# Kernel optimization log

Hardware: AMD Instinct MI355X
Metric: run time of the kernel (lower is better)

## Reference

```python
import jax, jax.numpy as jnp
import numpy as np

LN_EPS = 1e-5
LEAKY_SLOPE = 0.2

B, N_FEAT = 512, 8192
N_GROUPS, G, D = 512, 64, 128


def setup_inputs() -> dict:
    key = jax.random.key(0)
    k1, k2, k3 = jax.random.split(key, 3)
    x = jax.random.normal(k1, (B, N_FEAT), dtype=jnp.float32)
    idx = jax.random.randint(k2, (N_GROUPS, G), 0, N_FEAT)
    # per-group Linear weights, scaled like torch default init ~U(-1/sqrt(fan_in),...)
    W = jax.random.normal(k3, (N_GROUPS, G, D), dtype=jnp.float32) / jnp.sqrt(jnp.float32(G))
    b = jnp.zeros((N_GROUPS, D), dtype=jnp.float32)
    gamma = jnp.ones((D,), dtype=jnp.float32)   # shared LayerNorm affine (single nn.LayerNorm)
    beta = jnp.zeros((D,), dtype=jnp.float32)
    return {"x": x, "idx": idx, "W": W, "b": b, "gamma": gamma, "beta": beta}


def reference(x, idx, W, b, gamma, beta):
    # Gather each group's feature subset: [B, n_groups, G]
    xg = x[:, idx]
    # Grouped (block-diagonal) GEMM: per-group Linear -> [B, n_groups, D]
    h = jnp.einsum('bng,ngd->bnd', xg, W) + b
    # LeakyReLU(0.2)
    h = jnp.where(h >= 0, h, LEAKY_SLOPE * h)
    # Shared LayerNorm over last dim
    mu = jnp.mean(h, axis=-1, keepdims=True)
    c = h - mu
    var = jnp.mean(c * c, axis=-1, keepdims=True)
    out = c * jax.lax.rsqrt(var + LN_EPS) * gamma + beta
    # dropout treated as identity (deterministic/eval reference)
    return out  # matches torch.stack(output, dim=1): [B, n_groups, D]
```

## Files before the change

kernel.cpp:

```cpp
#include <hip/hip_runtime.h>
#include <stdint.h>

#define NB 512
#define NFEAT 8192
#define NG 512
#define GG 64
#define DD 128

typedef short bf16x8 __attribute__((ext_vector_type(8)));
typedef float f32x4 __attribute__((ext_vector_type(4)));
typedef unsigned int u32x4 __attribute__((ext_vector_type(4)));
typedef unsigned short u16;
typedef unsigned int u32;

__device__ __forceinline__ u16 f2bf(float f) {
  unsigned u = __builtin_bit_cast(unsigned, f);
  u += 0x7FFFu + ((u >> 16) & 1u);
  return (u16)(u >> 16);
}

__global__ __launch_bounds__(256) void prep_fused(const float* __restrict__ x,
                                                  u32* __restrict__ xTb32,
                                                  const float* __restrict__ W,
                                                  u16* __restrict__ Wt) {
  __shared__ __attribute__((aligned(16))) char lds[18432];
  const int bid = blockIdx.x;
  const int tid = threadIdx.x;
  if (bid < 1024) {
    float (*t)[65] = (float (*)[65])lds;
    const int c0 = (bid & 127) * 64;
    const int b0 = (bid >> 7) * 64;
    const int col = tid & 63;
    const int rg = tid >> 6;
    #pragma unroll
    for (int r = 0; r < 16; ++r) {
      int row = rg * 16 + r;
      t[col][row] = x[(size_t)(b0 + row) * NFEAT + c0 + col];
    }
    __syncthreads();
    const int sc = tid & 31;
    const int c = (sc & 15) + ((sc >> 4) << 5);
    const int srg = tid >> 5;
    #pragma unroll
    for (int r = 0; r < 8; ++r) {
      int crow = srg * 8 + r;
      unsigned px = (unsigned)f2bf(t[crow][c]) |
                    ((unsigned)f2bf(t[crow][c + 16]) << 16);
      xTb32[(size_t)(c0 + crow) * (NB / 2) + (b0 >> 1) + sc] = px;
    }
  } else {
    u16 (*tl)[GG + 8] = (u16 (*)[GG + 8])lds;
    const int n = bid - 1024;
    const float* wn = W + (size_t)n * (GG * DD);
    #pragma unroll
    for (int i = 0; i < 32; ++i) {
      int e = i * 256 + tid;
      int g = e >> 7, d = e & 127;
      tl[d][g] = f2bf(wn[e]);
    }
    __syncthreads();
    u16* dst = Wt + (size_t)n * (DD * GG);
    const int d = tid >> 1, gh = (tid & 1) * 32;
    const u16* src = &tl[d][gh];
    u32x4 v0 = *(const u32x4*)(src);
    u32x4 v1 = *(const u32x4*)(src + 8);
    u32x4 v2 = *(const u32x4*)(src + 16);
    u32x4 v3 = *(const u32x4*)(src + 24);
    u32x4* dp = (u32x4*)(dst + d * GG + gh);
    dp[0] = v0; dp[1] = v1; dp[2] = v2; dp[3] = v3;
  }
}

__global__ __launch_bounds__(256) void lc_mfma(
    const u32* __restrict__ xTb32,
    const u16* __restrict__ Wt,
    const int* __restrict__ idx,
    const float* __restrict__ bias,
    const float* __restrict__ gamma,
    const float* __restrict__ beta,
    float* __restrict__ out) {
  __shared__ __attribute__((aligned(16))) float ot[64][130];

  const int lin = blockIdx.x;
  const int xcd = lin & 7;
  const int slot = lin >> 3;
  const int n = (slot & 63) * 8 + xcd;
  const int b0 = (slot >> 6) * 128;
  const int tid = threadIdx.x;
  const int lane = tid & 63;
  const int w = tid >> 6;
  const int q = lane >> 4;
  const int lm = lane & 15;
  const int bb = b0 + w * 32;

  const int* idxn = idx + n * GG;

  int cof[16];
  #pragma unroll
  for (int ks = 0; ks < 2; ++ks) {
    int4 ca = *(const int4*)(idxn + ks * 32 + q * 8);
    int4 cb = *(const int4*)(idxn + ks * 32 + q * 8 + 4);
    cof[ks * 8 + 0] = ca.x * (NB / 2); cof[ks * 8 + 1] = ca.y * (NB / 2);
    cof[ks * 8 + 2] = ca.z * (NB / 2); cof[ks * 8 + 3] = ca.w * (NB / 2);
    cof[ks * 8 + 4] = cb.x * (NB / 2); cof[ks * 8 + 5] = cb.y * (NB / 2);
    cof[ks * 8 + 6] = cb.z * (NB / 2); cof[ks * 8 + 7] = cb.w * (NB / 2);
  }

  const int pairbase = (bb >> 1) + lm;
  bf16x8 afr[2][2];
  #pragma unroll
  for (int ks = 0; ks < 2; ++ks) {
    u32 d_[8];
    #pragma unroll
    for (int e = 0; e < 8; ++e)
      d_[e] = xTb32[(size_t)cof[ks * 8 + e] + pairbase];
    unsigned p0[4], p1[4];
    #pragma unroll
    for (int r = 0; r < 4; ++r) {
      u32 a = d_[2 * r], b = d_[2 * r + 1];
      p0[r] = (a & 0xffffu) | (b << 16);
      p1[r] = (a >> 16) | (b & 0xffff0000u);
    }
    u32x4 a4; a4.x = p0[0]; a4.y = p0[1]; a4.z = p0[2]; a4.w = p0[3];
    afr[ks][0] = __builtin_bit_cast(bf16x8, a4);
    u32x4 b4; b4.x = p1[0]; b4.y = p1[1]; b4.z = p1[2]; b4.w = p1[3];
    afr[ks][1] = __builtin_bit_cast(bf16x8, b4);
  }

  const u16* wtn = Wt + (size_t)n * (DD * GG);
  f32x4 acc[2][8];
  #pragma unroll
  for (int mi = 0; mi < 2; ++mi)
    #pragma unroll
    for (int ni = 0; ni < 8; ++ni) acc[mi][ni] = f32x4{0.f, 0.f, 0.f, 0.f};

  #pragma unroll
  for (int ks = 0; ks < 2; ++ks) {
    #pragma unroll
    for (int ni = 0; ni < 8; ++ni) {
      const int d = ni * 16 + lm;
      bf16x8 bfr = *(const bf16x8*)(wtn + d * GG + ks * 32 + q * 8);
      acc[0][ni] = __builtin_amdgcn_mfma_f32_16x16x32_bf16(afr[ks][0], bfr, acc[0][ni], 0, 0, 0);
      acc[1][ni] = __builtin_amdgcn_mfma_f32_16x16x32_bf16(afr[ks][1], bfr, acc[1][ni], 0, 0, 0);
    }
  }

  float bv[8], gv[8], tv[8];
  #pragma unroll
  for (int ni = 0; ni < 8; ++ni) {
    const int d = ni * 16 + lm;
    bv[ni] = bias[n * DD + d];
    gv[ni] = gamma[d];
    tv[ni] = beta[d];
  }
  const int hv = lane >> 5;
  const int dl = (lane & 31) * 4;
  #pragma unroll
  for (int mi = 0; mi < 2; ++mi) {
    #pragma unroll
    for (int r = 0; r < 4; ++r) {
      float h[8];
      float s = 0.f, s2 = 0.f;
      #pragma unroll
      for (int ni = 0; ni < 8; ++ni) {
        float v = acc[mi][ni][r] + bv[ni];
        v = (v >= 0.f) ? v : 0.2f * v;
        h[ni] = v;
        s += v;
        s2 += v * v;
      }
      s  += __shfl_xor(s, 1);  s  += __shfl_xor(s, 2);
      s  += __shfl_xor(s, 4);  s  += __shfl_xor(s, 8);
      s2 += __shfl_xor(s2, 1); s2 += __shfl_xor(s2, 2);
      s2 += __shfl_xor(s2, 4); s2 += __shfl_xor(s2, 8);
      const float mu = s * (1.f / 128.f);
      const float var = s2 * (1.f / 128.f) - mu * mu;
      const float rs = rsqrtf(var + 1e-5f);

      float* orow = &ot[w * 16 + q * 4 + r][lm];
      #pragma unroll
      for (int ni = 0; ni < 8; ++ni)
        orow[ni * 16] = (h[ni] - mu) * rs * gv[ni] + tv[ni];
    }
    __syncthreads();
    #pragma unroll
    for (int i = 0; i < 8; ++i) {
      const int rho = i * 8 + w * 2 + hv;
      const int grow = b0 + (rho >> 4) * 32 + mi * 16 + (rho & 15);
      f32x4 v = *(const f32x4*)&ot[rho][dl];
      __builtin_nontemporal_store(v, (f32x4*)(out + ((size_t)grow * NG + n) * DD + dl));
    }
    __syncthreads();
  }
}

extern "C" void kernel_launch(void* const* d_in, const int* in_sizes, int n_in,
                              void* d_out, int out_size, void* d_ws, size_t ws_size,
                              hipStream_t stream) {
  const float* x     = (const float*)d_in[0];
  const int*   idx   = (const int*)d_in[1];
  const float* W     = (const float*)d_in[2];
  const float* bias  = (const float*)d_in[3];
  const float* gamma = (const float*)d_in[4];
  const float* beta  = (const float*)d_in[5];
  float* out = (float*)d_out;

  u32* xTb32 = (u32*)d_ws;
  u16* Wt = (u16*)(xTb32 + (size_t)NFEAT * (NB / 2));

  prep_fused<<<1536, 256, 0, stream>>>(x, xTb32, W, Wt);
  lc_mfma<<<2048, 256, 0, stream>>>(xTb32, Wt, idx, bias, gamma, beta, out);
}
```

Before: 51.66 us.

## Process two batch tiles per block with gather prefetch overlapping epilogue

```diff
diff --git a/kernel.cpp b/kernel.cpp
--- a/kernel.cpp
+++ b/kernel.cpp
@@ -85,15 +85,17 @@
   const int xcd = lin & 7;
   const int slot = lin >> 3;
   const int n = (slot & 63) * 8 + xcd;
-  const int b0 = (slot >> 6) * 128;
+  const int b0s = (slot >> 6) * 256;
   const int tid = threadIdx.x;
   const int lane = tid & 63;
   const int w = tid >> 6;
   const int q = lane >> 4;
   const int lm = lane & 15;
-  const int bb = b0 + w * 32;
+  const int hv = lane >> 5;
+  const int dl = (lane & 31) * 4;
 
   const int* idxn = idx + n * GG;
+  const u16* wtn = Wt + (size_t)n * (DD * GG);
 
   int cof[16];
   #pragma unroll
@@ -106,44 +108,39 @@
     cof[ks * 8 + 6] = cb.z * (NB / 2); cof[ks * 8 + 7] = cb.w * (NB / 2);
   }
 
-  const int pairbase = (bb >> 1) + lm;
-  bf16x8 afr[2][2];
-  #pragma unroll
-  for (int ks = 0; ks < 2; ++ks) {
-    u32 d_[8];
-    #pragma unroll
-    for (int e = 0; e < 8; ++e)
-      d_[e] = xTb32[(size_t)cof[ks * 8 + e] + pairbase];
-    unsigned p0[4], p1[4];
-    #pragma unroll
-    for (int r = 0; r < 4; ++r) {
-      u32 a = d_[2 * r], b = d_[2 * r + 1];
-      p0[r] = (a & 0xffffu) | (b << 16);
-      p1[r] = (a >> 16) | (b & 0xffff0000u);
-    }
-    u32x4 a4; a4.x = p0[0]; a4.y = p0[1]; a4.z = p0[2]; a4.w = p0[3];
-    afr[ks][0] = __builtin_bit_cast(bf16x8, a4);
-    u32x4 b4; b4.x = p1[0]; b4.y = p1[1]; b4.z = p1[2]; b4.w = p1[3];
-    afr[ks][1] = __builtin_bit_cast(bf16x8, b4);
-  }
-
-  const u16* wtn = Wt + (size_t)n * (DD * GG);
-  f32x4 acc[2][8];
-  #pragma unroll
-  for (int mi = 0; mi < 2; ++mi)
-    #pragma unroll
-    for (int ni = 0; ni < 8; ++ni) acc[mi][ni] = f32x4{0.f, 0.f, 0.f, 0.f};
-
-  #pragma unroll
-  for (int ks = 0; ks < 2; ++ks) {
-    #pragma unroll
-    for (int ni = 0; ni < 8; ++ni) {
-      const int d = ni * 16 + lm;
-      bf16x8 bfr = *(const bf16x8*)(wtn + d * GG + ks * 32 + q * 8);
-      acc[0][ni] = __builtin_amdgcn_mfma_f32_16x16x32_bf16(afr[ks][0], bfr, acc[0][ni], 0, 0, 0);
-      acc[1][ni] = __builtin_amdgcn_mfma_f32_16x16x32_bf16(afr[ks][1], bfr, acc[1][ni], 0, 0, 0);
-    }
-  }
+  auto gather = [&](u32 (&d_)[16], int pairbase) {
+    #pragma unroll
+    for (int e = 0; e < 16; ++e)
+      d_[e] = xTb32[(size_t)cof[e] + pairbase];
+  };
+
+  auto pass_mfma = [&](const u32 (&d_)[16], f32x4 (&acc)[2][8]) {
+    #pragma unroll
+    for (int mi = 0; mi < 2; ++mi)
+      #pragma unroll
+      for (int ni = 0; ni < 8; ++ni) acc[mi][ni] = f32x4{0.f, 0.f, 0.f, 0.f};
+    #pragma unroll
+    for (int ks = 0; ks < 2; ++ks) {
+      unsigned p0[4], p1[4];
+      #pragma unroll
+      for (int r = 0; r < 4; ++r) {
+        u32 a = d_[ks * 8 + 2 * r], b = d_[ks * 8 + 2 * r + 1];
+        p0[r] = (a & 0xffffu) | (b << 16);
+        p1[r] = (a >> 16) | (b & 0xffff0000u);
+      }
+      u32x4 a4; a4.x = p0[0]; a4.y = p0[1]; a4.z = p0[2]; a4.w = p0[3];
+      bf16x8 af0 = __builtin_bit_cast(bf16x8, a4);
+      u32x4 b4; b4.x = p1[0]; b4.y = p1[1]; b4.z = p1[2]; b4.w = p1[3];
+      bf16x8 af1 = __builtin_bit_cast(bf16x8, b4);
+      #pragma unroll
+      for (int ni = 0; ni < 8; ++ni) {
+        const int d = ni * 16 + lm;
+        bf16x8 bfr = *(const bf16x8*)(wtn + d * GG + ks * 32 + q * 8);
+        acc[0][ni] = __builtin_amdgcn_mfma_f32_16x16x32_bf16(af0, bfr, acc[0][ni], 0, 0, 0);
+        acc[1][ni] = __builtin_amdgcn_mfma_f32_16x16x32_bf16(af1, bfr, acc[1][ni], 0, 0, 0);
+      }
+    }
+  };
 
   float bv[8], gv[8], tv[8];
   #pragma unroll
@@ -153,45 +150,55 @@
     gv[ni] = gamma[d];
     tv[ni] = beta[d];
   }
-  const int hv = lane >> 5;
-  const int dl = (lane & 31) * 4;
-  #pragma unroll
-  for (int mi = 0; mi < 2; ++mi) {
-    #pragma unroll
-    for (int r = 0; r < 4; ++r) {
-      float h[8];
-      float s = 0.f, s2 = 0.f;
-      #pragma unroll
-      for (int ni = 0; ni < 8; ++ni) {
-        float v = acc[mi][ni][r] + bv[ni];
-        v = (v >= 0.f) ? v : 0.2f * v;
-        h[ni] = v;
-        s += v;
-        s2 += v * v;
-      }
-      s  += __shfl_xor(s, 1);  s  += __shfl_xor(s, 2);
-      s  += __shfl_xor(s, 4);  s  += __shfl_xor(s, 8);
-      s2 += __shfl_xor(s2, 1); s2 += __shfl_xor(s2, 2);
-      s2 += __shfl_xor(s2, 4); s2 += __shfl_xor(s2, 8);
-      const float mu = s * (1.f / 128.f);
-      const float var = s2 * (1.f / 128.f) - mu * mu;
-      const float rs = rsqrtf(var + 1e-5f);
-
-      float* orow = &ot[w * 16 + q * 4 + r][lm];
-      #pragma unroll
-      for (int ni = 0; ni < 8; ++ni)
-        orow[ni * 16] = (h[ni] - mu) * rs * gv[ni] + tv[ni];
-    }
-    __syncthreads();
-    #pragma unroll
-    for (int i = 0; i < 8; ++i) {
-      const int rho = i * 8 + w * 2 + hv;
-      const int grow = b0 + (rho >> 4) * 32 + mi * 16 + (rho & 15);
-      f32x4 v = *(const f32x4*)&ot[rho][dl];
-      __builtin_nontemporal_store(v, (f32x4*)(out + ((size_t)grow * NG + n) * DD + dl));
-    }
-    __syncthreads();
-  }
+
+  auto epilogue = [&](f32x4 (&acc)[2][8], int bbp) {
+    #pragma unroll
+    for (int mi = 0; mi < 2; ++mi) {
+      #pragma unroll
+      for (int r = 0; r < 4; ++r) {
+        float h[8];
+        float s = 0.f, s2 = 0.f;
+        #pragma unroll
+        for (int ni = 0; ni < 8; ++ni) {
+          float v = acc[mi][ni][r] + bv[ni];
+          v = (v >= 0.f) ? v : 0.2f * v;
+          h[ni] = v;
+          s += v;
+          s2 += v * v;
+        }
+        s  += __shfl_xor(s, 1);  s  += __shfl_xor(s, 2);
+        s  += __shfl_xor(s, 4);  s  += __shfl_xor(s, 8);
+        s2 += __shfl_xor(s2, 1); s2 += __shfl_xor(s2, 2);
+        s2 += __shfl_xor(s2, 4); s2 += __shfl_xor(s2, 8);
+        const float mu = s * (1.f / 128.f);
+        const float var = s2 * (1.f / 128.f) - mu * mu;
+        const float rs = rsqrtf(var + 1e-5f);
+        float* orow = &ot[w * 16 + q * 4 + r][lm];
+        #pragma unroll
+        for (int ni = 0; ni < 8; ++ni)
+          orow[ni * 16] = (h[ni] - mu) * rs * gv[ni] + tv[ni];
+      }
+      __syncthreads();
+      #pragma unroll
+      for (int i = 0; i < 8; ++i) {
+        const int rho = i * 8 + w * 2 + hv;
+        const int grow = bbp + (rho >> 4) * 32 + mi * 16 + (rho & 15);
+        f32x4 v = *(const f32x4*)&ot[rho][dl];
+        __builtin_nontemporal_store(v, (f32x4*)(out + ((size_t)grow * NG + n) * DD + dl));
+      }
+      __syncthreads();
+    }
+  };
+
+  u32 d1_[16], d2_[16];
+  gather(d1_, ((b0s + w * 32) >> 1) + lm);
+  f32x4 acc[2][8];
+  pass_mfma(d1_, acc);
+  gather(d2_, ((b0s + 128 + w * 32) >> 1) + lm);
+  epilogue(acc, b0s);
+
+  pass_mfma(d2_, acc);
+  epilogue(acc, b0s + 128);
 }
 
 extern "C" void kernel_launch(void* const* d_in, const int* in_sizes, int n_in,
@@ -209,5 +216,5 @@
   u16* Wt = (u16*)(xTb32 + (size_t)NFEAT * (NB / 2));
 
   prep_fused<<<1536, 256, 0, stream>>>(x, xTb32, W, Wt);
-  lc_mfma<<<2048, 256, 0, stream>>>(xTb32, Wt, idx, bias, gamma, beta, out);
-}
+  lc_mfma<<<1024, 256, 0, stream>>>(xTb32, Wt, idx, bias, gamma, beta, out);
+}
```

Result: no change. 51.66 us (median of 2 runs) (+0.0%).
